# Performance work log

Hardware: AMD Instinct MI355X
Metric: run time of the kernel (lower is better)

Reference implementation:

```python
import jax, jax.numpy as jnp
import numpy as np

S = 10      # num_synapse
D = 32      # num_dendrite
L = 4       # num_layers
B = 1024    # batch
M = 2 ** S - 1  # mask rows


def _make_mask():
    # rows are binary expansions of 1..2^S-1, MSB first (bin(x).zfill)
    buf = [[int(c) for c in bin(v)[2:].zfill(S)] for v in range(1, 2 ** S)]
    return jnp.asarray(np.array(buf, dtype=np.float32))  # (M, S)

_MASK = _make_mask()


def setup_inputs() -> dict:
    key = jax.random.key(0)
    ks_ = jax.random.split(key, 6)
    x = jax.random.uniform(ks_[0], (B, 1, S), dtype=jnp.float32)
    k = jnp.ones((L, D, S), jnp.float32) * 10.0
    pb = jax.random.uniform(ks_[1], (L, D, S), dtype=jnp.float32) - 0.5
    w = pb * 2.0
    q = pb * 1.0
    bnd_m = 1.0 / np.sqrt(M)
    dend_w = jax.random.uniform(ks_[2], (L, M), jnp.float32, -bnd_m, bnd_m)
    dend_b = jax.random.uniform(ks_[3], (L,), jnp.float32, -bnd_m, bnd_m)
    bnd_d = 1.0 / np.sqrt(D)
    lin_w = jax.random.uniform(ks_[4], (L, D), jnp.float32, -bnd_d, bnd_d)
    lin_b = jax.random.uniform(ks_[5], (L,), jnp.float32, -bnd_d, bnd_d)
    bnd_l = 1.0 / np.sqrt(L)
    final_w = jax.random.uniform(jax.random.fold_in(key, 7), (L,), jnp.float32, -bnd_l, bnd_l)
    final_b = jax.random.uniform(jax.random.fold_in(key, 8), (1,), jnp.float32, -bnd_l, bnd_l)
    ks = jnp.ones((1,), jnp.float32) * 10.0
    return {"x": x, "k": k, "w": w, "q": q, "dend_w": dend_w, "dend_b": dend_b,
            "lin_w": lin_w, "lin_b": lin_b, "final_w": final_w, "final_b": final_b, "ks": ks}


def reference(x, k, w, q, dend_w, dend_b, lin_w, lin_b, final_w, final_b, ks):
    # x: (B,1,S) -> broadcast against per-layer (L,D,S) params -> (B,L,D,S)
    s = jax.nn.sigmoid(k[None] * (w[None] * x[:, None] - q[None]))  # (B,L,D,S), s>0
    # prod_s s^mask == exp(mask @ log s): fused power+product reduction
    feat = jnp.exp(jnp.einsum('blds,ms->bldm', jnp.log(s), _MASK))  # (B,L,D,M)
    dend = jnp.einsum('bldm,lm->bld', feat, dend_w) + dend_b[None, :, None]  # per-layer Linear(M,1)
    out = jnp.einsum('bld,ld->bl', dend, lin_w) + lin_b[None]  # per-layer Linear(D,1) (num_soma=1)
    fin = out @ final_w + final_b  # Linear(L,1) -> (B,)
    return jax.nn.sigmoid(ks * fin)  # (B,)
```

## Files before the change

kernel.cpp:

```cpp
#include <hip/hip_runtime.h>
#include <hip/hip_bf16.h>


#define NS 10

__global__ __launch_bounds__(256) void dendrite_fwd(
    const float* __restrict__ x,
    const float* __restrict__ k,
    const float* __restrict__ w,
    const float* __restrict__ q,
    const float* __restrict__ dend_w,
    const float* __restrict__ dend_b,
    const float* __restrict__ lin_w,
    const float* __restrict__ lin_b,
    const float* __restrict__ final_w,
    const float* __restrict__ final_b,
    const float* __restrict__ ks,
    float* __restrict__ out)
{
    const int lane = threadIdx.x & 63;
    const int wv   = threadIdx.x >> 6;
    const int l    = __builtin_amdgcn_readfirstlane(wv);
    const int d    = lane & 31;
    const int bl   = lane >> 5;
    const int b    = blockIdx.x * 2 + bl;

    const float* kp = k + (l * 32 + d) * NS;
    const float* wp = w + (l * 32 + d) * NS;
    const float* qp = q + (l * 32 + d) * NS;
    const float* xp = x + b * NS;

    float t[NS];
#pragma unroll
    for (int i = 0; i < NS; ++i) {
        float z = kp[i] * (wp[i] * xp[i] - qp[i]);
        float s = 1.0f / (1.0f + __expf(-z));
        t[NS - 1 - i] = s;
    }

    float pl[32], ph[32];
    pl[0] = 1.0f;
    ph[0] = 1.0f;
#pragma unroll
    for (int v = 1; v < 32; ++v) {
        pl[v] = pl[v & (v - 1)] * t[__builtin_ctz(v)];
        ph[v] = ph[v & (v - 1)] * t[5 + __builtin_ctz(v)];
    }

    const float* dw = dend_w + l * 1023;

    float acc;
    {
        float i0 = 0.f, i1 = 0.f, i2 = 0.f, i3 = 0.f;
#pragma unroll
        for (int vl = 1; vl < 32; vl += 4) {
            i0 = fmaf(dw[vl - 1], pl[vl], i0);
            if (vl + 1 < 32) i1 = fmaf(dw[vl + 0], pl[vl + 1], i1);
            if (vl + 2 < 32) i2 = fmaf(dw[vl + 1], pl[vl + 2], i2);
            if (vl + 3 < 32) i3 = fmaf(dw[vl + 2], pl[vl + 3], i3);
        }
        acc = (i0 + i1) + (i2 + i3);
    }
#pragma unroll
    for (int vh = 1; vh < 32; ++vh) {
        const float* dwr = dw + vh * 32 - 1;
        float i0 = 0.f, i1 = 0.f, i2 = 0.f, i3 = 0.f;
#pragma unroll
        for (int j = 0; j < 8; ++j) {
            i0 = fmaf(dwr[4 * j + 0], pl[4 * j + 0], i0);
            i1 = fmaf(dwr[4 * j + 1], pl[4 * j + 1], i1);
            i2 = fmaf(dwr[4 * j + 2], pl[4 * j + 2], i2);
            i3 = fmaf(dwr[4 * j + 3], pl[4 * j + 3], i3);
        }
        acc = fmaf(ph[vh], (i0 + i1) + (i2 + i3), acc);
    }

    float contrib = (acc + dend_b[l]) * lin_w[l * 32 + d];
#pragma unroll
    for (int off = 16; off >= 1; off >>= 1)
        contrib += __shfl_xor(contrib, off, 64);

    __shared__ float red[4][2];
    if (d == 0)
        red[wv][bl] = (contrib + lin_b[l]) * final_w[l];
    __syncthreads();

    if (threadIdx.x < 2) {
        float fin = red[0][threadIdx.x] + red[1][threadIdx.x] +
                    red[2][threadIdx.x] + red[3][threadIdx.x] + final_b[0];
        out[blockIdx.x * 2 + threadIdx.x] = 1.0f / (1.0f + __expf(-ks[0] * fin));
    }
}

extern "C" void kernel_launch(void* const* d_in, const int* in_sizes, int n_in,
                              void* d_out, int out_size, void* d_ws, size_t ws_size,
                              hipStream_t stream) {
    const float* x       = (const float*)d_in[0];
    const float* k       = (const float*)d_in[1];
    const float* w       = (const float*)d_in[2];
    const float* q       = (const float*)d_in[3];
    const float* dend_w  = (const float*)d_in[4];
    const float* dend_b  = (const float*)d_in[5];
    const float* lin_w   = (const float*)d_in[6];
    const float* lin_b   = (const float*)d_in[7];
    const float* final_w = (const float*)d_in[8];
    const float* final_b = (const float*)d_in[9];
    const float* ksp     = (const float*)d_in[10];
    float* out           = (float*)d_out;

    dendrite_fwd<<<512, 256, 0, stream>>>(x, k, w, q, dend_w, dend_b,
                                          lin_w, lin_b, final_w, final_b,
                                          ksp, out);
}
```

Baseline: 83.91 us.

## Stage dend_w in LDS and split high-bit products across half-waves

Each block now copies the whole dend_w table (4 layers x 1023) into shared memory, padded to 1024 per layer so that rows align for float4 LDS reads. The kernel then handles one batch element per block, with the two half-waves each covering half of the high-bit subsets (16 rows each). The two halves are combined with a wider shuffle reduction, and the bias is halved to avoid counting it twice. This swaps scalar global/constant loads of the weight table for vectorized LDS reads and halves per-thread FMA work, but each of the now 1024 blocks pays a 16 KB table copy plus an extra barrier.

New measurement: 80.52 us. 4.0% less time.

```diff
diff --git a/kernel.cpp b/kernel.cpp
--- a/kernel.cpp
+++ b/kernel.cpp
@@ -18,12 +18,27 @@
     const float* __restrict__ ks,
     float* __restrict__ out)
 {
-    const int lane = threadIdx.x & 63;
-    const int wv   = threadIdx.x >> 6;
+    __shared__ float dwl[4 * 1024];
+    __shared__ float red[4];
+
+    const int tid  = threadIdx.x;
+    const int lane = tid & 63;
+    const int wv   = tid >> 6;
     const int l    = __builtin_amdgcn_readfirstlane(wv);
     const int d    = lane & 31;
-    const int bl   = lane >> 5;
-    const int b    = blockIdx.x * 2 + bl;
+    const int h    = lane >> 5;
+    const int b    = blockIdx.x;
+
+    if (tid < 4) dwl[tid * 1024] = 0.0f;
+#pragma unroll
+    for (int it = 0; it < 16; ++it) {
+        int j = tid + it * 256;
+        if (j < 4 * 1023) {
+            int lj = j / 1023;
+            int r  = j - lj * 1023;
+            dwl[lj * 1024 + r + 1] = dend_w[j];
+        }
+    }
 
     const float* kp = k + (l * 32 + d) * NS;
     const float* wp = w + (l * 32 + d) * NS;
@@ -34,61 +49,51 @@
 #pragma unroll
     for (int i = 0; i < NS; ++i) {
         float z = kp[i] * (wp[i] * xp[i] - qp[i]);
-        float s = 1.0f / (1.0f + __expf(-z));
-        t[NS - 1 - i] = s;
+        t[NS - 1 - i] = 1.0f / (1.0f + __expf(-z));
     }
 
-    float pl[32], ph[32];
+    float pl[32];
     pl[0] = 1.0f;
-    ph[0] = 1.0f;
 #pragma unroll
-    for (int v = 1; v < 32; ++v) {
+    for (int v = 1; v < 32; ++v)
         pl[v] = pl[v & (v - 1)] * t[__builtin_ctz(v)];
-        ph[v] = ph[v & (v - 1)] * t[5 + __builtin_ctz(v)];
-    }
 
-    const float* dw = dend_w + l * 1023;
+    float ph[16];
+    ph[0] = h ? t[9] : 1.0f;
+#pragma unroll
+    for (int u = 1; u < 16; ++u)
+        ph[u] = ph[u & (u - 1)] * t[5 + __builtin_ctz(u)];
 
-    float acc;
-    {
-        float i0 = 0.f, i1 = 0.f, i2 = 0.f, i3 = 0.f;
+    __syncthreads();
+
+    const float4* row4 = (const float4*)(dwl + l * 1024 + h * 16 * 32);
+    float acc = 0.0f;
 #pragma unroll
-        for (int vl = 1; vl < 32; vl += 4) {
-            i0 = fmaf(dw[vl - 1], pl[vl], i0);
-            if (vl + 1 < 32) i1 = fmaf(dw[vl + 0], pl[vl + 1], i1);
-            if (vl + 2 < 32) i2 = fmaf(dw[vl + 1], pl[vl + 2], i2);
-            if (vl + 3 < 32) i3 = fmaf(dw[vl + 2], pl[vl + 3], i3);
-        }
-        acc = (i0 + i1) + (i2 + i3);
-    }
-#pragma unroll
-    for (int vh = 1; vh < 32; ++vh) {
-        const float* dwr = dw + vh * 32 - 1;
+    for (int u = 0; u < 16; ++u) {
         float i0 = 0.f, i1 = 0.f, i2 = 0.f, i3 = 0.f;
 #pragma unroll
         for (int j = 0; j < 8; ++j) {
-            i0 = fmaf(dwr[4 * j + 0], pl[4 * j + 0], i0);
-            i1 = fmaf(dwr[4 * j + 1], pl[4 * j + 1], i1);
-            i2 = fmaf(dwr[4 * j + 2], pl[4 * j + 2], i2);
-            i3 = fmaf(dwr[4 * j + 3], pl[4 * j + 3], i3);
+            float4 c = row4[u * 8 + j];
+            i0 = fmaf(c.x, pl[4 * j + 0], i0);
+            i1 = fmaf(c.y, pl[4 * j + 1], i1);
+            i2 = fmaf(c.z, pl[4 * j + 2], i2);
+            i3 = fmaf(c.w, pl[4 * j + 3], i3);
         }
-        acc = fmaf(ph[vh], (i0 + i1) + (i2 + i3), acc);
+        acc = fmaf(ph[u], (i0 + i1) + (i2 + i3), acc);
     }
 
-    float contrib = (acc + dend_b[l]) * lin_w[l * 32 + d];
+    float contrib = (acc + 0.5f * dend_b[l]) * lin_w[l * 32 + d];
 #pragma unroll
-    for (int off = 16; off >= 1; off >>= 1)
+    for (int off = 32; off >= 1; off >>= 1)
         contrib += __shfl_xor(contrib, off, 64);
 
-    __shared__ float red[4][2];
-    if (d == 0)
-        red[wv][bl] = (contrib + lin_b[l]) * final_w[l];
+    if (lane == 0)
+        red[wv] = (contrib + lin_b[l]) * final_w[l];
     __syncthreads();
 
-    if (threadIdx.x < 2) {
-        float fin = red[0][threadIdx.x] + red[1][threadIdx.x] +
-                    red[2][threadIdx.x] + red[3][threadIdx.x] + final_b[0];
-        out[blockIdx.x * 2 + threadIdx.x] = 1.0f / (1.0f + __expf(-ks[0] * fin));
+    if (tid == 0) {
+        float fin = red[0] + red[1] + red[2] + red[3] + final_b[0];
+        out[b] = 1.0f / (1.0f + __expf(-ks[0] * fin));
     }
 }
 
@@ -108,7 +113,7 @@
     const float* ksp     = (const float*)d_in[10];
     float* out           = (float*)d_out;
 
-    dendrite_fwd<<<512, 256, 0, stream>>>(x, k, w, q, dend_w, dend_b,
-                                          lin_w, lin_b, final_w, final_b,
-                                          ksp, out);
+    dendrite_fwd<<<1024, 256, 0, stream>>>(x, k, w, q, dend_w, dend_b,
+                                           lin_w, lin_b, final_w, final_b,
+                                           ksp, out);
 }
```
